# Optimization experiments

Measured on AMD Instinct MI355X. Metric: run time of the kernel, lower is better.

Reference implementation:

```python
import jax, jax.numpy as jnp
import numpy as np
from jax import lax

B, N, FD, D, H, LH, HC, NC = 8, 1024, 34, 64, 4, 128, 193, 9
STEPS, ET = 4, 2
DH = D // H
LHH = LH // 2  # hidden per LSTM direction
SCALE = float(1.0 / np.sqrt(DH))
BN_INV = float(1.0 / np.sqrt(1.0 + 1e-5))  # BatchNorm eval with running var=1


def layernorm(x, g, b, eps=1e-5):
    m = x.mean(-1, keepdims=True)
    v = ((x - m) ** 2).mean(-1, keepdims=True)
    return (x - m) / jnp.sqrt(v + eps) * g + b


def mha(q_in, kv, w, b, ow, ob):
    # torch nn.MultiheadAttention, batch_first, eval (no dropout)
    wq, wk, wv = jnp.split(w, 3, 0)
    bq, bk, bv = jnp.split(b, 3, 0)
    q = (q_in @ wq.T + bq).reshape(B, N, H, DH)
    k = (kv @ wk.T + bk).reshape(B, N, H, DH)
    v = (kv @ wv.T + bv).reshape(B, N, H, DH)
    s = jnp.einsum('bqhd,bkhd->bhqk', q, k) * SCALE
    a = jax.nn.softmax(s, -1)
    o = jnp.einsum('bhqk,bkhd->bqhd', a, v).reshape(B, N, D)
    return o @ ow.T + ob


def gru(x, h, wih, whh, bih, bhh):
    gi = x @ wih.T + bih
    gh = h @ whh.T + bhh
    ir, iz, inn = jnp.split(gi, 3, -1)
    hr, hz, hn = jnp.split(gh, 3, -1)
    r = jax.nn.sigmoid(ir + hr)
    z = jax.nn.sigmoid(iz + hz)
    n = jnp.tanh(inn + r * hn)
    return (1.0 - z) * n + z * h


def lstm_dir(x, wih, whh, b, reverse):
    hd = wih.shape[0] // 4
    def step(carry, xt):
        h, c = carry
        g = xt @ wih.T + h @ whh.T + b
        i, f, gg, o = jnp.split(g, 4, -1)
        c = jax.nn.sigmoid(f) * c + jax.nn.sigmoid(i) * jnp.tanh(gg)
        h = jax.nn.sigmoid(o) * jnp.tanh(c)
        return (h, c), h
    xs = jnp.swapaxes(x, 0, 1)
    if reverse:
        xs = xs[::-1]
    z0 = jnp.zeros((x.shape[0], hd), x.dtype)
    (hf, _), hs = lax.scan(step, (z0, z0), xs)
    if reverse:
        hs = hs[::-1]
    return jnp.swapaxes(hs, 0, 1), hf


def forward(node_features, adj_data, adj_control, handcrafted_features,
            ip_w, ip_b, et_w, mha_in_w, mha_in_b, mha_out_w, mha_out_b,
            eta_w1, eta_b1, eta_w2, eta_b2, gru_wih, gru_whh, gru_bih, gru_bhh,
            ln_g, ln_b, oln_g, oln_b,
            l0f_wih, l0f_whh, l0f_b, l0b_wih, l0b_whh, l0b_b,
            l1f_wih, l1f_whh, l1f_b, l1b_wih, l1b_whh, l1b_b,
            attn_w1, attn_b1, attn_w2, attn_b2,
            hc_w1, hc_b1, bn1_g, bn1_b, hc_w2, hc_b2, bn2_g, bn2_b, hc_w3, hc_b3,
            cls_w1, cls_b1, cls_w2, cls_b2, cls_w3, cls_b3,
            topo_order, node_mask, seq_lengths):
    # input projection
    h = jax.nn.relu(node_features @ ip_w.T + ip_b)
    adjs = (adj_data, adj_control)
    for l in range(STEPS):
        msgs = []
        for e in range(ET):
            ht = h @ et_w[l, e].T
            m = mha(h, ht, mha_in_w[l, e], mha_in_b[l, e], mha_out_w[l, e], mha_out_b[l, e])
            msgs.append(jnp.einsum('bij,bjd->bid', adjs[e], m))
        st = jnp.stack(msgs, 2)            # [B,N,ET,D]
        ctx = st.mean(2)
        ai = jnp.concatenate([h, ctx], -1)
        etw = jax.nn.softmax(jax.nn.relu(ai @ eta_w1[l].T + eta_b1[l]) @ eta_w2[l].T + eta_b2[l], -1)
        messages = (st * etw[..., None]).sum(2)
        hn = gru(messages, h, gru_wih[l], gru_whh[l], gru_bih[l], gru_bhh[l])
        hn = layernorm(hn, ln_g[l], ln_b[l])
        h = layernorm(h + hn, oln_g[l], oln_b[l])
    h = h * node_mask.astype(h.dtype)[..., None]
    h_ord = jnp.take_along_axis(h, topo_order[..., None], 1)
    # 2-layer BiLSTM
    o0f, _ = lstm_dir(h_ord, l0f_wih, l0f_whh, l0f_b, False)
    o0b, _ = lstm_dir(h_ord, l0b_wih, l0b_whh, l0b_b, True)
    o0 = jnp.concatenate([o0f, o0b], -1)
    o1f, h1f = lstm_dir(o0, l1f_wih, l1f_whh, l1f_b, False)
    o1b, h1b = lstm_dir(o0, l1b_wih, l1b_whh, l1b_b, True)
    h_all = jnp.concatenate([o1f, o1b], -1)    # [B,N,LH]
    final = jnp.concatenate([h1f, h1b], -1)    # [B,LH]
    # masked attention pooling
    scores = (jnp.tanh(h_all @ attn_w1.T + attn_b1) @ attn_w2.T + attn_b2)[..., 0]
    smask = jnp.arange(N)[None, :] < seq_lengths[:, None]
    aw = jax.nn.softmax(jnp.where(smask, scores, -1e9), -1)
    pooled = jnp.einsum('bt,btd->bd', aw, h_all)
    comb = pooled + final
    # handcrafted encoder (BN in eval mode, running stats 0/1)
    x = jax.nn.relu(handcrafted_features @ hc_w1.T + hc_b1)
    x = x * BN_INV * bn1_g + bn1_b
    x = jax.nn.relu(x @ hc_w2.T + hc_b2)
    x = x * BN_INV * bn2_g + bn2_b
    x = jax.nn.relu(x @ hc_w3.T + hc_b3)
    hf = jnp.concatenate([comb, x], -1)
    y = jax.nn.relu(hf @ cls_w1.T + cls_b1)
    y = jax.nn.relu(y @ cls_w2.T + cls_b2)
    return y @ cls_w3.T + cls_b3


def setup_inputs():
    key = jax.random.key(0)
    ks = iter(jax.random.split(key, 128))
    def rn(shape, s=0.05):
        return (jax.random.normal(next(ks), shape) * s).astype(jnp.float32)
    inp = {}
    inp['node_features'] = jax.random.normal(next(ks), (B, N, FD), jnp.float32)
    inp['adj_data'] = jax.random.uniform(next(ks), (B, N, N), jnp.float32) * (2.0 / N)
    inp['adj_control'] = jax.random.uniform(next(ks), (B, N, N), jnp.float32) * (2.0 / N)
    inp['handcrafted_features'] = jax.random.normal(next(ks), (B, HC), jnp.float32)
    inp['ip_w'] = rn((D, FD)); inp['ip_b'] = rn((D,))
    inp['et_w'] = rn((STEPS, ET, D, D))
    inp['mha_in_w'] = rn((STEPS, ET, 3 * D, D)); inp['mha_in_b'] = rn((STEPS, ET, 3 * D))
    inp['mha_out_w'] = rn((STEPS, ET, D, D)); inp['mha_out_b'] = rn((STEPS, ET, D))
    inp['eta_w1'] = rn((STEPS, D, 2 * D)); inp['eta_b1'] = rn((STEPS, D))
    inp['eta_w2'] = rn((STEPS, ET, D)); inp['eta_b2'] = rn((STEPS, ET))
    inp['gru_wih'] = rn((STEPS, 3 * D, D)); inp['gru_whh'] = rn((STEPS, 3 * D, D))
    inp['gru_bih'] = rn((STEPS, 3 * D)); inp['gru_bhh'] = rn((STEPS, 3 * D))
    inp['ln_g'] = jnp.ones((STEPS, D), jnp.float32); inp['ln_b'] = jnp.zeros((STEPS, D), jnp.float32)
    inp['oln_g'] = jnp.ones((STEPS, D), jnp.float32); inp['oln_b'] = jnp.zeros((STEPS, D), jnp.float32)
    inp['l0f_wih'] = rn((4 * LHH, D)); inp['l0f_whh'] = rn((4 * LHH, LHH)); inp['l0f_b'] = rn((4 * LHH,))
    inp['l0b_wih'] = rn((4 * LHH, D)); inp['l0b_whh'] = rn((4 * LHH, LHH)); inp['l0b_b'] = rn((4 * LHH,))
    inp['l1f_wih'] = rn((4 * LHH, LH)); inp['l1f_whh'] = rn((4 * LHH, LHH)); inp['l1f_b'] = rn((4 * LHH,))
    inp['l1b_wih'] = rn((4 * LHH, LH)); inp['l1b_whh'] = rn((4 * LHH, LHH)); inp['l1b_b'] = rn((4 * LHH,))
    inp['attn_w1'] = rn((64, LH)); inp['attn_b1'] = rn((64,))
    inp['attn_w2'] = rn((1, 64)); inp['attn_b2'] = rn((1,))
    inp['hc_w1'] = rn((256, HC)); inp['hc_b1'] = rn((256,))
    inp['bn1_g'] = jnp.ones((256,), jnp.float32); inp['bn1_b'] = jnp.zeros((256,), jnp.float32)
    inp['hc_w2'] = rn((128, 256)); inp['hc_b2'] = rn((128,))
    inp['bn2_g'] = jnp.ones((128,), jnp.float32); inp['bn2_b'] = jnp.zeros((128,), jnp.float32)
    inp['hc_w3'] = rn((64, 128)); inp['hc_b3'] = rn((64,))
    inp['cls_w1'] = rn((128, LH + 64)); inp['cls_b1'] = rn((128,))
    inp['cls_w2'] = rn((64, 128)); inp['cls_b2'] = rn((64,))
    inp['cls_w3'] = rn((NC, 64)); inp['cls_b3'] = rn((NC,))
    inp['topo_order'] = jax.vmap(lambda k: jax.random.permutation(k, N))(jax.random.split(next(ks), B))
    inp['node_mask'] = jnp.ones((B, N), bool)
    inp['seq_lengths'] = jax.random.randint(next(ks), (B,), N // 2, N + 1)
    return inp


def reference(node_features, adj_data, adj_control, handcrafted_features,
              ip_w, ip_b, et_w, mha_in_w, mha_in_b, mha_out_w, mha_out_b,
              eta_w1, eta_b1, eta_w2, eta_b2, gru_wih, gru_whh, gru_bih, gru_bhh,
              ln_g, ln_b, oln_g, oln_b,
              l0f_wih, l0f_whh, l0f_b, l0b_wih, l0b_whh, l0b_b,
              l1f_wih, l1f_whh, l1f_b, l1b_wih, l1b_whh, l1b_b,
              attn_w1, attn_b1, attn_w2, attn_b2,
              hc_w1, hc_b1, bn1_g, bn1_b, hc_w2, hc_b2, bn2_g, bn2_b, hc_w3, hc_b3,
              cls_w1, cls_b1, cls_w2, cls_b2, cls_w3, cls_b3,
              topo_order, node_mask, seq_lengths):
    return forward(node_features, adj_data, adj_control, handcrafted_features,
                   ip_w, ip_b, et_w, mha_in_w, mha_in_b, mha_out_w, mha_out_b,
                   eta_w1, eta_b1, eta_w2, eta_b2, gru_wih, gru_whh, gru_bih, gru_bhh,
                   ln_g, ln_b, oln_g, oln_b,
                   l0f_wih, l0f_whh, l0f_b, l0b_wih, l0b_whh, l0b_b,
                   l1f_wih, l1f_whh, l1f_b, l1b_wih, l1b_whh, l1b_b,
                   attn_w1, attn_b1, attn_w2, attn_b2,
                   hc_w1, hc_b1, bn1_g, bn1_b, hc_w2, hc_b2, bn2_g, bn2_b, hc_w3, hc_b3,
                   cls_w1, cls_b1, cls_w2, cls_b2, cls_w3, cls_b3,
                   topo_order, node_mask, seq_lengths)
```

## Files before the change

kernel.cpp:

```cpp
#include <hip/hip_runtime.h>
#include <math.h>

#define NB 8
#define NN 1024
#define NT 8192
#define SCALE_C 0.25f
#define BN_INV_C 0.99999500003749969f
#define LN_EPS 1e-5f

typedef __attribute__((ext_vector_type(8))) short bf16x8;
typedef __attribute__((ext_vector_type(4))) float f32x4;

__device__ __forceinline__ float sigmoidf_(float x){ return 1.f/(1.f+__expf(-x)); }
__device__ __forceinline__ float tanhf_(float x){
  float ax = fabsf(x);
  float e = __expf(-2.f*ax);
  float t = (1.f-e)/(1.f+e);
  return x < 0.f ? -t : t;
}
__device__ __forceinline__ float wsum64(float v){
  #pragma unroll
  for (int m=1; m<64; m<<=1) v += __shfl_xor(v, m);
  return v;
}
__device__ __forceinline__ unsigned short f2bf(float f){
  unsigned int u = __float_as_uint(f);
  unsigned int r = (u + 0x7fffu + ((u>>16)&1u)) >> 16;
  return (unsigned short)r;
}

__global__ __launch_bounds__(256) void gemm_tn(
    const float* __restrict__ A, long aZ,
    const float* __restrict__ W, long wZ,
    const float* __restrict__ Bias, long bZ,
    float* __restrict__ C, long cZ,
    int M, int Ncols, int K, int act)
{
  const int z = blockIdx.z;
  A += (long)z * aZ; W += (long)z * wZ; C += (long)z * cZ;
  if (Bias) Bias += (long)z * bZ;
  const int m0 = blockIdx.x * 64;
  const int n0 = blockIdx.y * 64;
  const int tid = threadIdx.x;
  __shared__ float As[16][68];
  __shared__ float Ws[16][68];
  const int lm = tid >> 2;
  const int kq = (tid & 3) * 4;
  const int tr = tid >> 4;
  const int tc = tid & 15;
  float acc[4][4] = {};
  const bool v16 = ((K & 15) == 0);
  for (int kt = 0; kt < K; kt += 16) {
    if (v16) {
      float4 a = *reinterpret_cast<const float4*>(&A[(long)(m0 + lm) * K + kt + kq]);
      As[kq+0][lm]=a.x; As[kq+1][lm]=a.y; As[kq+2][lm]=a.z; As[kq+3][lm]=a.w;
      float4 w = *reinterpret_cast<const float4*>(&W[(long)(n0 + lm) * K + kt + kq]);
      Ws[kq+0][lm]=w.x; Ws[kq+1][lm]=w.y; Ws[kq+2][lm]=w.z; Ws[kq+3][lm]=w.w;
    } else {
      #pragma unroll
      for (int j = 0; j < 4; ++j) {
        int k = kt + kq + j;
        As[kq+j][lm] = (k < K) ? A[(long)(m0+lm)*K + k] : 0.f;
        Ws[kq+j][lm] = (k < K) ? W[(long)(n0+lm)*K + k] : 0.f;
      }
    }
    __syncthreads();
    #pragma unroll
    for (int k = 0; k < 16; ++k) {
      float4 av = *reinterpret_cast<const float4*>(&As[k][tr*4]);
      float4 wv = *reinterpret_cast<const float4*>(&Ws[k][tc*4]);
      float a_[4] = {av.x,av.y,av.z,av.w};
      float w_[4] = {wv.x,wv.y,wv.z,wv.w};
      #pragma unroll
      for (int i=0;i<4;++i)
        #pragma unroll
        for (int j=0;j<4;++j) acc[i][j] += a_[i]*w_[j];
    }
    __syncthreads();
  }
  #pragma unroll
  for (int i=0;i<4;++i) {
    const long m = m0 + tr*4 + i;
    #pragma unroll
    for (int j=0;j<4;++j) {
      const int n = n0 + tc*4 + j;
      float v = acc[i][j];
      if (Bias) v += Bias[n];
      if (act) v = fmaxf(v, 0.f);
      C[m*Ncols + n] = v;
    }
  }
}

__global__ __launch_bounds__(256) void wprep(
    const float* __restrict__ miw, const float* __restrict__ etw,
    float* __restrict__ wcomb)
{
  const int le = blockIdx.x;
  const float* Wm = miw + (long)le*192*64;
  const float* Et = etw + (long)le*64*64;
  float* Out = wcomb + (long)le*192*64;
  __shared__ float es[64][65];
  const int tid = threadIdx.x;
  for (int i = tid; i < 4096; i += 256) es[i>>6][i&63] = Et[i];
  __syncthreads();
  for (int i = tid; i < 4096; i += 256) Out[i] = Wm[i];
  for (int i = tid; i < 8192; i += 256) {
    const int r = 64 + (i >> 6), d = i & 63;
    const float* wr = &Wm[(long)r*64];
    float a = 0.f;
    #pragma unroll 8
    for (int c = 0; c < 64; ++c) a += wr[c] * es[c][d];
    Out[(long)r*64 + d] = a;
  }
}

__global__ __launch_bounds__(256) void mcvt_kernel(
    const float* __restrict__ m0, const float* __restrict__ m1,
    unsigned short* __restrict__ mmT)
{
  const int e = blockIdx.y;
  const float* src = e ? m1 : m0;
  unsigned short* dst = mmT + (long)e*64*8192;
  const int r0 = blockIdx.x * 64;
  __shared__ unsigned short tile[64][65];
  const int tid = threadIdx.x;
  const int lr = tid >> 2, c0 = (tid & 3) * 16;
  #pragma unroll
  for (int i = 0; i < 16; i += 4) {
    float4 v = *reinterpret_cast<const float4*>(&src[(long)(r0+lr)*64 + c0 + i]);
    tile[lr][c0+i+0] = f2bf(v.x);
    tile[lr][c0+i+1] = f2bf(v.y);
    tile[lr][c0+i+2] = f2bf(v.z);
    tile[lr][c0+i+3] = f2bf(v.w);
  }
  __syncthreads();
  const int n = tid >> 2, rr = (tid & 3) * 16;
  #pragma unroll
  for (int i = 0; i < 16; i += 4) {
    ushort4 w;
    w.x = tile[rr+i+0][n];
    w.y = tile[rr+i+1][n];
    w.z = tile[rr+i+2][n];
    w.w = tile[rr+i+3][n];
    *reinterpret_cast<ushort4*>(&dst[(long)n*8192 + r0 + rr + i]) = w;
  }
}

__global__ __launch_bounds__(256) void gemm_nn_mfma(
    const float* __restrict__ adjD, const float* __restrict__ adjC,
    const unsigned short* __restrict__ mmT,
    float* __restrict__ msg)
{
  const int z = blockIdx.z;
  const int e = z >> 3, b = z & 7;
  const float* A = (e ? adjC : adjD) + (long)b*NN*NN;
  const unsigned short* Bt = mmT + (long)e*64*8192 + (long)b*NN;
  float* Cp = msg + ((long)e*NT + (long)b*NN) * 64;
  const int tid = threadIdx.x;
  const int w = tid >> 6;
  const int l = tid & 63;
  const int r = l & 15;
  const int kg = l >> 4;
  const long arow = (long)(blockIdx.x*64 + w*16 + r) * NN;

  f32x4 acc0 = {0.f,0.f,0.f,0.f}, acc1 = acc0, acc2 = acc0, acc3 = acc0;

  for (int k0 = 0; k0 < NN; k0 += 32) {
    const float4* ap = reinterpret_cast<const float4*>(&A[arow + k0 + kg*8]);
    float4 a0 = ap[0], a1 = ap[1];
    union { unsigned short us[8]; bf16x8 v; } au;
    au.us[0]=f2bf(a0.x); au.us[1]=f2bf(a0.y); au.us[2]=f2bf(a0.z); au.us[3]=f2bf(a0.w);
    au.us[4]=f2bf(a1.x); au.us[5]=f2bf(a1.y); au.us[6]=f2bf(a1.z); au.us[7]=f2bf(a1.w);
    bf16x8 b0 = *reinterpret_cast<const bf16x8*>(&Bt[(long)(0*16+r)*8192 + k0 + kg*8]);
    bf16x8 b1 = *reinterpret_cast<const bf16x8*>(&Bt[(long)(1*16+r)*8192 + k0 + kg*8]);
    bf16x8 b2 = *reinterpret_cast<const bf16x8*>(&Bt[(long)(2*16+r)*8192 + k0 + kg*8]);
    bf16x8 b3 = *reinterpret_cast<const bf16x8*>(&Bt[(long)(3*16+r)*8192 + k0 + kg*8]);
    acc0 = __builtin_amdgcn_mfma_f32_16x16x32_bf16(au.v, b0, acc0, 0, 0, 0);
    acc1 = __builtin_amdgcn_mfma_f32_16x16x32_bf16(au.v, b1, acc1, 0, 0, 0);
    acc2 = __builtin_amdgcn_mfma_f32_16x16x32_bf16(au.v, b2, acc2, 0, 0, 0);
    acc3 = __builtin_amdgcn_mfma_f32_16x16x32_bf16(au.v, b3, acc3, 0, 0, 0);
  }
  const int crow = blockIdx.x*64 + w*16 + kg*4;
  #pragma unroll
  for (int i = 0; i < 4; ++i) {
    Cp[(long)(crow+i)*64 + 0*16 + r] = acc0[i];
    Cp[(long)(crow+i)*64 + 1*16 + r] = acc1[i];
    Cp[(long)(crow+i)*64 + 2*16 + r] = acc2[i];
    Cp[(long)(crow+i)*64 + 3*16 + r] = acc3[i];
  }
}

__global__ __launch_bounds__(256) void attn_kernel(
    const float* __restrict__ qkv, float* __restrict__ O)
{
  const int e = blockIdx.z;
  const float* base = qkv + (long)e*1572864;
  float* o = O + (long)e*524288;
  const int bh = blockIdx.y;
  const int b = bh >> 2, head = bh & 3;
  const int q0 = blockIdx.x * 64;
  const int tid = threadIdx.x;
  const int r = tid >> 2, p = tid & 3;
  const long row = (long)b*NN + q0 + r;
  float qreg[16];
  {
    const float4* qp = reinterpret_cast<const float4*>(&base[row*192 + head*16]);
    #pragma unroll
    for (int i=0;i<4;++i) {
      float4 v = qp[i];
      qreg[4*i+0]=v.x*SCALE_C; qreg[4*i+1]=v.y*SCALE_C;
      qreg[4*i+2]=v.z*SCALE_C; qreg[4*i+3]=v.w*SCALE_C;
    }
  }
  float mx = -1e30f, ssum = 0.f, acc[16];
  #pragma unroll
  for (int d=0;d<16;++d) acc[d]=0.f;
  __shared__ float ks[128][17];
  __shared__ float vs[128][17];
  for (int j0 = 0; j0 < NN; j0 += 128) {
    {
      const int jr = tid >> 1;
      const int hf = (tid & 1) * 8;
      const long rr = ((long)b*NN + j0 + jr)*192 + head*16 + hf;
      const float4* kp = reinterpret_cast<const float4*>(&base[rr + 64]);
      float4 k0 = kp[0], k1 = kp[1];
      ks[jr][hf+0]=k0.x; ks[jr][hf+1]=k0.y; ks[jr][hf+2]=k0.z; ks[jr][hf+3]=k0.w;
      ks[jr][hf+4]=k1.x; ks[jr][hf+5]=k1.y; ks[jr][hf+6]=k1.z; ks[jr][hf+7]=k1.w;
      const float4* vp = reinterpret_cast<const float4*>(&base[rr + 128]);
      float4 v0 = vp[0], v1 = vp[1];
      vs[jr][hf+0]=v0.x; vs[jr][hf+1]=v0.y; vs[jr][hf+2]=v0.z; vs[jr][hf+3]=v0.w;
      vs[jr][hf+4]=v1.x; vs[jr][hf+5]=v1.y; vs[jr][hf+6]=v1.z; vs[jr][hf+7]=v1.w;
    }
    __syncthreads();
    for (int jj = p; jj < 128; jj += 4) {
      float s = 0.f;
      #pragma unroll
      for (int d=0;d<16;++d) s += qreg[d]*ks[jj][d];
      if (s <= mx) {
        float ee = __expf(s - mx);
        ssum += ee;
        #pragma unroll
        for (int d=0;d<16;++d) acc[d] += ee*vs[jj][d];
      } else {
        float cc = __expf(mx - s);
        ssum = ssum*cc + 1.f;
        #pragma unroll
        for (int d=0;d<16;++d) acc[d] = acc[d]*cc + vs[jj][d];
        mx = s;
      }
    }
    __syncthreads();
  }
  #pragma unroll
  for (int mask=1; mask<=2; mask<<=1) {
    float om = __shfl_xor(mx, mask);
    float os = __shfl_xor(ssum, mask);
    float nm = fmaxf(mx, om);
    float c1 = __expf(mx-nm), c2 = __expf(om-nm);
    ssum = ssum*c1 + os*c2;
    #pragma unroll
    for (int d=0;d<16;++d) {
      float ov = __shfl_xor(acc[d], mask);
      acc[d] = acc[d]*c1 + ov*c2;
    }
    mx = nm;
  }
  if (p == 0) {
    float inv = 1.f/ssum;
    float4* op = reinterpret_cast<float4*>(&o[row*64 + head*16]);
    #pragma unroll
    for (int i=0;i<4;++i) {
      float4 v;
      v.x=acc[4*i+0]*inv; v.y=acc[4*i+1]*inv; v.z=acc[4*i+2]*inv; v.w=acc[4*i+3]*inv;
      op[i] = v;
    }
  }
}

__global__ __launch_bounds__(64) void fused_gate_gru_ln(
    float* __restrict__ h, const float* __restrict__ msg0, const float* __restrict__ msg1,
    const float* __restrict__ ew1, const float* __restrict__ eb1,
    const float* __restrict__ ew2, const float* __restrict__ eb2,
    const float* __restrict__ wih, const float* __restrict__ whh,
    const float* __restrict__ bih, const float* __restrict__ bhh,
    const float* __restrict__ lng, const float* __restrict__ lnb,
    const float* __restrict__ olng, const float* __restrict__ olnb)
{
  const int r0 = blockIdx.x * 4;
  const int tid = threadIdx.x;
  __shared__ float hsm[4][64], m0s[4][64], m1s[4][64], tss[4][64];
  #pragma unroll
  for (int r=0;r<4;++r) {
    hsm[r][tid] = h[(long)(r0+r)*64 + tid];
    m0s[r][tid] = msg0[(long)(r0+r)*64 + tid];
    m1s[r][tid] = msg1[(long)(r0+r)*64 + tid];
  }
  __syncthreads();
  float ta[4] = {0.f,0.f,0.f,0.f};
  for (int k=0;k<64;++k) {
    float w = ew1[tid*128 + k];
    #pragma unroll
    for (int r=0;r<4;++r) ta[r] += w * hsm[r][k];
  }
  for (int k=0;k<64;++k) {
    float w = ew1[tid*128 + 64 + k];
    #pragma unroll
    for (int r=0;r<4;++r) ta[r] += w * 0.5f*(m0s[r][k]+m1s[r][k]);
  }
  #pragma unroll
  for (int r=0;r<4;++r) tss[r][tid] = fmaxf(ta[r] + eb1[tid], 0.f);
  __syncthreads();
  const float w2a = ew2[tid], w2b = ew2[64+tid];
  #pragma unroll
  for (int r=0;r<4;++r) {
    float l0 = wsum64(tss[r][tid]*w2a) + eb2[0];
    float l1 = wsum64(tss[r][tid]*w2b) + eb2[1];
    float mm = fmaxf(l0,l1);
    float e0 = __expf(l0-mm), e1 = __expf(l1-mm);
    float wgt0 = e0/(e0+e1);
    m0s[r][tid] = wgt0*m0s[r][tid] + (1.f-wgt0)*m1s[r][tid];
  }
  __syncthreads();
  float air[4]={},aiz[4]={},ain[4]={},ahr[4]={},ahz[4]={},ahn[4]={};
  for (int k=0;k<64;++k) {
    float wir = wih[(long)tid*64 + k];
    float wiz = wih[(long)(64+tid)*64 + k];
    float win = wih[(long)(128+tid)*64 + k];
    float whr = whh[(long)tid*64 + k];
    float whz = whh[(long)(64+tid)*64 + k];
    float whn = whh[(long)(128+tid)*64 + k];
    #pragma unroll
    for (int r=0;r<4;++r) {
      float x = m0s[r][k], hh = hsm[r][k];
      air[r] += wir*x; aiz[r] += wiz*x; ain[r] += win*x;
      ahr[r] += whr*hh; ahz[r] += whz*hh; ahn[r] += whn*hh;
    }
  }
  const float bir = bih[tid], biz = bih[64+tid], bin_ = bih[128+tid];
  const float bhr = bhh[tid], bhz = bhh[64+tid], bhn = bhh[128+tid];
  const float g1 = lng[tid], b1v = lnb[tid], g2 = olng[tid], b2v = olnb[tid];
  #pragma unroll
  for (int r=0;r<4;++r) {
    float rg = sigmoidf_(air[r]+bir + ahr[r]+bhr);
    float zg = sigmoidf_(aiz[r]+biz + ahz[r]+bhz);
    float ng = tanhf_(ain[r]+bin_ + rg*(ahn[r]+bhn));
    float hnv = (1.f-zg)*ng + zg*hsm[r][tid];
    float mu = wsum64(hnv) * 0.015625f;
    float dv = hnv - mu;
    float var = wsum64(dv*dv) * 0.015625f;
    float y = dv * rsqrtf(var + LN_EPS) * g1 + b1v;
    float ho = hsm[r][tid] + y;
    float mu2 = wsum64(ho) * 0.015625f;
    float d2 = ho - mu2;
    float var2 = wsum64(d2*d2) * 0.015625f;
    h[(long)(r0+r)*64 + tid] = d2 * rsqrtf(var2 + LN_EPS) * g2 + b2v;
  }
}

__global__ __launch_bounds__(256) void permute_kernel(
    const float* __restrict__ h, const int* __restrict__ topo, float* __restrict__ ho)
{
  const long idx = (long)blockIdx.x*256 + threadIdx.x;
  const int row = (int)(idx >> 6), d = (int)(idx & 63);
  const int b = row >> 10, i = row & 1023;
  const int src = topo[b*1024 + i];
  ho[idx] = h[((long)b*1024 + src)*64 + d];
}

__global__ __launch_bounds__(256) void lstm_seq(
    const float* __restrict__ xpF, const float* __restrict__ xpB,
    const float* __restrict__ whhF, const float* __restrict__ whhB,
    float* __restrict__ out)
{
  const int b = blockIdx.x;
  const int dir = blockIdx.y;
  const float* xp = dir ? xpB : xpF;
  const float* W  = dir ? whhB : whhF;
  const int colOff = dir * 64;
  const int tid = threadIdx.x;
  const int wv  = tid >> 6;
  const int j   = tid & 63;

  float4 wreg[16];
  {
    const float4* wp = reinterpret_cast<const float4*>(&W[tid*64]);
    #pragma unroll
    for (int i=0;i<16;++i) wreg[i] = wp[i];
  }

  __shared__ __align__(16) float hs[2][64];
  __shared__ float g5[2][320];
  float c = 0.f;
  if (tid < 64) hs[0][tid] = 0.f;

  int ts = dir ? (NN-1) : 0;
  float xnext = xp[((long)b*NN + ts)*256 + tid];
  __syncthreads();

  int p = 0;
  for (int t = 0; t < NN; ++t) {
    const int cur = ts;
    const float x = xnext;
    if (t + 1 < NN) {
      ts = dir ? (NN-2-t) : (t+1);
      xnext = xp[((long)b*NN + ts)*256 + tid];
    }
    float a0 = x, a1 = 0.f, a2 = 0.f, a3 = 0.f;
    #pragma unroll
    for (int k=0;k<16;k+=4) {
      float4 h0 = *reinterpret_cast<const float4*>(&hs[p][k*4]);
      float4 h1 = *reinterpret_cast<const float4*>(&hs[p][k*4+4]);
      float4 h2 = *reinterpret_cast<const float4*>(&hs[p][k*4+8]);
      float4 h3 = *reinterpret_cast<const float4*>(&hs[p][k*4+12]);
      a0 += wreg[k].x*h0.x + wreg[k].y*h0.y + wreg[k].z*h0.z + wreg[k].w*h0.w;
      a1 += wreg[k+1].x*h1.x + wreg[k+1].y*h1.y + wreg[k+1].z*h1.z + wreg[k+1].w*h1.w;
      a2 += wreg[k+2].x*h2.x + wreg[k+2].y*h2.y + wreg[k+2].z*h2.z + wreg[k+2].w*h2.w;
      a3 += wreg[k+3].x*h3.x + wreg[k+3].y*h3.y + wreg[k+3].z*h3.z + wreg[k+3].w*h3.w;
    }
    float dot = (a0+a1)+(a2+a3);
    float v = (wv == 2) ? tanhf_(dot) : sigmoidf_(dot);
    g5[p][j*5 + wv] = v;
    __syncthreads();
    const float gi = g5[p][j*5+0];
    const float gf = g5[p][j*5+1];
    const float gg = g5[p][j*5+2];
    const float go = g5[p][j*5+3];
    c = gf*c + gi*gg;
    const float hval = go * tanhf_(c);
    hs[p^1][j] = hval;
    if (tid < 64) out[((long)b*NN + cur)*128 + colOff + j] = hval;
    p ^= 1;
  }
}

__global__ __launch_bounds__(64) void score_kernel(
    const float* __restrict__ h_all, const float* __restrict__ w1,
    const float* __restrict__ b1, const float* __restrict__ w2,
    const float* __restrict__ b2, float* __restrict__ scores)
{
  const int row = blockIdx.x, tid = threadIdx.x;
  __shared__ float xs[128];
  xs[tid]    = h_all[(long)row*128 + tid];
  xs[64+tid] = h_all[(long)row*128 + 64 + tid];
  __syncthreads();
  float a = b1[tid];
  for (int k=0;k<128;++k) a += w1[tid*128+k]*xs[k];
  float s = tanhf_(a) * w2[tid];
  s = wsum64(s);
  if (tid==0) scores[row] = s + b2[0];
}

__global__ __launch_bounds__(256) void pool_kernel(
    const float* __restrict__ h_all, const float* __restrict__ scores,
    const int* __restrict__ seqlen, float* __restrict__ comb)
{
  const int b = blockIdx.x, tid = threadIdx.x;
  __shared__ float aw[1024];
  __shared__ float red[4];
  __shared__ float part[256];
  const int L = seqlen[b];
  float mx = -1e30f;
  for (int t = tid; t < 1024; t += 256) {
    float s = (t < L) ? scores[b*1024+t] : -1e30f;
    aw[t] = s;
    mx = fmaxf(mx, s);
  }
  #pragma unroll
  for (int m=1;m<64;m<<=1) mx = fmaxf(mx, __shfl_xor(mx,m));
  if ((tid&63)==0) red[tid>>6] = mx;
  __syncthreads();
  mx = fmaxf(fmaxf(red[0],red[1]), fmaxf(red[2],red[3]));
  __syncthreads();
  float ss = 0.f;
  for (int t = tid; t < 1024; t += 256) {
    float e = (t < L) ? __expf(aw[t]-mx) : 0.f;
    aw[t] = e; ss += e;
  }
  ss = wsum64(ss);
  if ((tid&63)==0) red[tid>>6] = ss;
  __syncthreads();
  ss = red[0]+red[1]+red[2]+red[3];
  const float inv = 1.f/ss;
  const int d = tid & 127, hseg = tid >> 7;
  float acc = 0.f;
  for (int t = hseg; t < 1024; t += 2)
    acc += aw[t] * h_all[((long)b*1024 + t)*128 + d];
  part[tid] = acc;
  __syncthreads();
  if (tid < 128) {
    float pooled = (part[tid] + part[tid+128]) * inv;
    float fin = (tid < 64) ? h_all[((long)b*1024 + 1023)*128 + tid]
                           : h_all[((long)b*1024 + 0)*128 + tid];
    comb[b*128 + tid] = pooled + fin;
  }
}

__global__ __launch_bounds__(256) void head_kernel(
    const float* __restrict__ comb, const float* __restrict__ hcf,
    const float* __restrict__ w1, const float* __restrict__ b1,
    const float* __restrict__ bn1g, const float* __restrict__ bn1b,
    const float* __restrict__ w2, const float* __restrict__ b2,
    const float* __restrict__ bn2g, const float* __restrict__ bn2b,
    const float* __restrict__ w3, const float* __restrict__ b3,
    const float* __restrict__ cw1, const float* __restrict__ cb1,
    const float* __restrict__ cw2, const float* __restrict__ cb2,
    const float* __restrict__ cw3, const float* __restrict__ cb3,
    float* __restrict__ outp)
{
  const int b = blockIdx.x, tid = threadIdx.x;
  __shared__ float hrow[193];
  __shared__ float x1[256], x2[128], hf[192], y1[128], y2[64];
  if (tid < 193) hrow[tid] = hcf[b*193 + tid];
  if (tid < 128) hf[tid] = comb[b*128 + tid];
  __syncthreads();
  {
    float a = b1[tid];
    for (int k=0;k<193;++k) a += w1[(long)tid*193+k]*hrow[k];
    x1[tid] = fmaxf(a,0.f)*BN_INV_C*bn1g[tid] + bn1b[tid];
  }
  __syncthreads();
  if (tid < 128) {
    float a = b2[tid];
    for (int k=0;k<256;++k) a += w2[(long)tid*256+k]*x1[k];
    x2[tid] = fmaxf(a,0.f)*BN_INV_C*bn2g[tid] + bn2b[tid];
  }
  __syncthreads();
  if (tid < 64) {
    float a = b3[tid];
    for (int k=0;k<128;++k) a += w3[(long)tid*128+k]*x2[k];
    hf[128+tid] = fmaxf(a,0.f);
  }
  __syncthreads();
  if (tid < 128) {
    float a = cb1[tid];
    for (int k=0;k<192;++k) a += cw1[(long)tid*192+k]*hf[k];
    y1[tid] = fmaxf(a,0.f);
  }
  __syncthreads();
  if (tid < 64) {
    float a = cb2[tid];
    for (int k=0;k<128;++k) a += cw2[(long)tid*128+k]*y1[k];
    y2[tid] = fmaxf(a,0.f);
  }
  __syncthreads();
  if (tid < 9) {
    float a = cb3[tid];
    for (int k=0;k<64;++k) a += cw3[(long)tid*64+k]*y2[k];
    outp[b*9+tid] = a;
  }
}

extern "C" void kernel_launch(void* const* d_in, const int* in_sizes, int n_in,
                              void* d_out, int out_size, void* d_ws, size_t ws_size,
                              hipStream_t stream)
{
  const float* nf   = (const float*)d_in[0];
  const float* adjD = (const float*)d_in[1];
  const float* adjC = (const float*)d_in[2];
  const float* hcf  = (const float*)d_in[3];
  const float* ip_w = (const float*)d_in[4];
  const float* ip_b = (const float*)d_in[5];
  const float* et_w = (const float*)d_in[6];
  const float* miw  = (const float*)d_in[7];
  const float* mib  = (const float*)d_in[8];
  const float* mow  = (const float*)d_in[9];
  const float* mob  = (const float*)d_in[10];
  const float* ew1  = (const float*)d_in[11];
  const float* eb1  = (const float*)d_in[12];
  const float* ew2  = (const float*)d_in[13];
  const float* eb2  = (const float*)d_in[14];
  const float* gwih = (const float*)d_in[15];
  const float* gwhh = (const float*)d_in[16];
  const float* gbih = (const float*)d_in[17];
  const float* gbhh = (const float*)d_in[18];
  const float* lng  = (const float*)d_in[19];
  const float* lnb  = (const float*)d_in[20];
  const float* olng = (const float*)d_in[21];
  const float* olnb = (const float*)d_in[22];
  const float* l0f_wih = (const float*)d_in[23];
  const float* l0f_whh = (const float*)d_in[24];
  const float* l0f_b   = (const float*)d_in[25];
  const float* l0b_wih = (const float*)d_in[26];
  const float* l0b_whh = (const float*)d_in[27];
  const float* l0b_b   = (const float*)d_in[28];
  const float* l1f_wih = (const float*)d_in[29];
  const float* l1f_whh = (const float*)d_in[30];
  const float* l1f_b   = (const float*)d_in[31];
  const float* l1b_wih = (const float*)d_in[32];
  const float* l1b_whh = (const float*)d_in[33];
  const float* l1b_b   = (const float*)d_in[34];
  const float* aw1  = (const float*)d_in[35];
  const float* ab1  = (const float*)d_in[36];
  const float* aw2  = (const float*)d_in[37];
  const float* ab2  = (const float*)d_in[38];
  const float* hw1  = (const float*)d_in[39];
  const float* hb1  = (const float*)d_in[40];
  const float* bn1g = (const float*)d_in[41];
  const float* bn1b = (const float*)d_in[42];
  const float* hw2  = (const float*)d_in[43];
  const float* hb2  = (const float*)d_in[44];
  const float* bn2g = (const float*)d_in[45];
  const float* bn2b = (const float*)d_in[46];
  const float* hw3  = (const float*)d_in[47];
  const float* hb3  = (const float*)d_in[48];
  const float* cw1  = (const float*)d_in[49];
  const float* cb1  = (const float*)d_in[50];
  const float* cw2  = (const float*)d_in[51];
  const float* cb2  = (const float*)d_in[52];
  const float* cw3  = (const float*)d_in[53];
  const float* cb3  = (const float*)d_in[54];
  const int*  topo  = (const int*)d_in[55];
  const int*  seqlen= (const int*)d_in[57];

  float* ws = (float*)d_ws;
  float* h     = ws;
  float* qkv   = ws + 524288;
  float* ob    = ws + 3670016;
  float* mbuf  = ws + 4718592;
  float* msg   = ws + 5767168;
  unsigned short* mmT = (unsigned short*)(ws + 6815744);
  float* wcomb = ws + 7340032;
  float* hord  = ws + 524288;
  float* xpf   = ws + 1048576;
  float* xpb   = ws + 3145728;
  float* o0    = ws + 5767168;
  float* hall  = ws + 7438336;
  float* sc    = ws + 8486912;
  float* comb  = ws + 8495104;

  dim3 blk(256);

  wprep<<<dim3(8), blk, 0, stream>>>(miw, et_w, wcomb);

  gemm_tn<<<dim3(128,1,1), blk, 0, stream>>>(nf,0, ip_w,0, ip_b,0, h,0, NT,64,34, 1);

  for (int l=0; l<4; ++l) {
    const float* mowl = mow + (size_t)l*2*64*64;
    const float* mobl = mob + (size_t)l*2*64;
    gemm_tn<<<dim3(128,3,2), blk, 0, stream>>>(h,0, wcomb + (size_t)l*2*12288, 12288,
                                               mib + (size_t)l*2*192, 192,
                                               qkv, 1572864, NT,192,64, 0);
    attn_kernel<<<dim3(16,32,2), blk, 0, stream>>>(qkv, ob);
    gemm_tn<<<dim3(128,1,2), blk, 0, stream>>>(ob,524288, mowl,4096, mobl,64, mbuf,524288, NT,64,64, 0);
    mcvt_kernel<<<dim3(128,2), blk, 0, stream>>>(mbuf, mbuf+524288, mmT);
    gemm_nn_mfma<<<dim3(16,1,16), blk, 0, stream>>>(adjD, adjC, mmT, msg);
    fused_gate_gru_ln<<<dim3(2048), dim3(64), 0, stream>>>(h, msg, msg+524288,
        ew1 + (size_t)l*64*128, eb1 + l*64, ew2 + l*128, eb2 + l*2,
        gwih + (size_t)l*192*64, gwhh + (size_t)l*192*64, gbih + l*192, gbhh + l*192,
        lng + l*64, lnb + l*64, olng + l*64, olnb + l*64);
  }

  permute_kernel<<<dim3(2048), blk, 0, stream>>>(h, topo, hord);

  gemm_tn<<<dim3(128,4,1), blk, 0, stream>>>(hord,0, l0f_wih,0, l0f_b,0, xpf,0, NT,256,64, 0);
  gemm_tn<<<dim3(128,4,1), blk, 0, stream>>>(hord,0, l0b_wih,0, l0b_b,0, xpb,0, NT,256,64, 0);
  lstm_seq<<<dim3(8,2), blk, 0, stream>>>(xpf, xpb, l0f_whh, l0b_whh, o0);
  gemm_tn<<<dim3(128,4,1), blk, 0, stream>>>(o0,0, l1f_wih,0, l1f_b,0, xpf,0, NT,256,128, 0);
  gemm_tn<<<dim3(128,4,1), blk, 0, stream>>>(o0,0, l1b_wih,0, l1b_b,0, xpb,0, NT,256,128, 0);
  lstm_seq<<<dim3(8,2), blk, 0, stream>>>(xpf, xpb, l1f_whh, l1b_whh, hall);

  score_kernel<<<dim3(8192), dim3(64), 0, stream>>>(hall, aw1, ab1, aw2, ab2, sc);
  pool_kernel<<<dim3(8), blk, 0, stream>>>(hall, sc, seqlen, comb);
  head_kernel<<<dim3(8), blk, 0, stream>>>(comb, hcf,
      hw1,hb1,bn1g,bn1b, hw2,hb2,bn2g,bn2b, hw3,hb3,
      cw1,cb1, cw2,cb2, cw3,cb3, (float*)d_out);
}
```

Baseline: 2.780 ms.

## Batch all sequences per LSTM direction into one block using fp16 MFMA recurrence

The LSTM recurrence kernel now runs one block per direction and processes all 8 batch sequences together. The hidden-to-gate product becomes fp16 16x16x32 MFMA operations, with weights held in registers as fp16 and the hidden state kept in a swizzled fp16 LDS buffer. This removes the per-step scalar FMA dot products and the gate-exchange LDS round trip, and each thread now handles all four gates for its units. The costs are fp16 rounding of the weights and hidden state in a 1024-step recurrence, and only 2 blocks running on the whole GPU.

```diff
diff --git a/kernel.cpp b/kernel.cpp
--- a/kernel.cpp
+++ b/kernel.cpp
@@ -10,6 +10,7 @@
 
 typedef __attribute__((ext_vector_type(8))) short bf16x8;
 typedef __attribute__((ext_vector_type(4))) float f32x4;
+typedef _Float16 f16x8 __attribute__((ext_vector_type(8)));
 
 __device__ __forceinline__ float sigmoidf_(float x){ return 1.f/(1.f+__expf(-x)); }
 __device__ __forceinline__ float tanhf_(float x){
@@ -373,63 +374,93 @@
     const float* __restrict__ whhF, const float* __restrict__ whhB,
     float* __restrict__ out)
 {
-  const int b = blockIdx.x;
-  const int dir = blockIdx.y;
+  const int dir = blockIdx.x;
   const float* xp = dir ? xpB : xpF;
   const float* W  = dir ? whhB : whhF;
   const int colOff = dir * 64;
   const int tid = threadIdx.x;
-  const int wv  = tid >> 6;
-  const int j   = tid & 63;
-
-  float4 wreg[16];
+  const int w   = tid >> 6;
+  const int l   = tid & 63;
+  const int col = l & 15;
+  const int bidx = col & 7;
+  const int kg  = l >> 4;
+  const int u0  = w*16 + kg*4;
+
+  f16x8 Wf[4][2];
+  #pragma unroll
+  for (int c=0;c<4;++c)
+    #pragma unroll
+    for (int s=0;s<2;++s) {
+      const float* wr = &W[(long)(c*64 + w*16 + col)*64 + s*32 + kg*8];
+      f16x8 f;
+      #pragma unroll
+      for (int j=0;j<8;++j) f[j] = (_Float16)wr[j];
+      Wf[c][s] = f;
+    }
+
+  __shared__ __align__(16) _Float16 hbuf[2][1024];
+  for (int i = tid; i < 1024; i += 256) hbuf[0][i] = (_Float16)0.f;
+  float cst[4] = {0.f,0.f,0.f,0.f};
+
+  const int swz    = (col & 7) << 4;
+  const int rdoff0 = col*128 + ((0*64 + kg*16) ^ swz);
+  const int rdoff1 = col*128 + ((1*64 + kg*16) ^ swz);
+  const int wroff  = col*128 + ((u0*2)        ^ swz);
+
+  int ts = dir ? (NN-1) : 0;
+  float4 xq[4];
   {
-    const float4* wp = reinterpret_cast<const float4*>(&W[tid*64]);
-    #pragma unroll
-    for (int i=0;i<16;++i) wreg[i] = wp[i];
-  }
-
-  __shared__ __align__(16) float hs[2][64];
-  __shared__ float g5[2][320];
-  float c = 0.f;
-  if (tid < 64) hs[0][tid] = 0.f;
-
-  int ts = dir ? (NN-1) : 0;
-  float xnext = xp[((long)b*NN + ts)*256 + tid];
+    const float* xr = &xp[((long)bidx*NN + ts)*256];
+    #pragma unroll
+    for (int c=0;c<4;++c)
+      xq[c] = *reinterpret_cast<const float4*>(&xr[c*64 + u0]);
+  }
   __syncthreads();
 
   int p = 0;
   for (int t = 0; t < NN; ++t) {
     const int cur = ts;
-    const float x = xnext;
+    const char* hb = (const char*)(&hbuf[p][0]);
+    f16x8 B0 = *reinterpret_cast<const f16x8*>(hb + rdoff0);
+    f16x8 B1 = *reinterpret_cast<const f16x8*>(hb + rdoff1);
+    f32x4 aI = {xq[0].x, xq[0].y, xq[0].z, xq[0].w};
+    f32x4 aF = {xq[1].x, xq[1].y, xq[1].z, xq[1].w};
+    f32x4 aG = {xq[2].x, xq[2].y, xq[2].z, xq[2].w};
+    f32x4 aO = {xq[3].x, xq[3].y, xq[3].z, xq[3].w};
     if (t + 1 < NN) {
       ts = dir ? (NN-2-t) : (t+1);
-      xnext = xp[((long)b*NN + ts)*256 + tid];
-    }
-    float a0 = x, a1 = 0.f, a2 = 0.f, a3 = 0.f;
-    #pragma unroll
-    for (int k=0;k<16;k+=4) {
-      float4 h0 = *reinterpret_cast<const float4*>(&hs[p][k*4]);
-      float4 h1 = *reinterpret_cast<const float4*>(&hs[p][k*4+4]);
-      float4 h2 = *reinterpret_cast<const float4*>(&hs[p][k*4+8]);
-      float4 h3 = *reinterpret_cast<const float4*>(&hs[p][k*4+12]);
-      a0 += wreg[k].x*h0.x + wreg[k].y*h0.y + wreg[k].z*h0.z + wreg[k].w*h0.w;
-      a1 += wreg[k+1].x*h1.x + wreg[k+1].y*h1.y + wreg[k+1].z*h1.z + wreg[k+1].w*h1.w;
-      a2 += wreg[k+2].x*h2.x + wreg[k+2].y*h2.y + wreg[k+2].z*h2.z + wreg[k+2].w*h2.w;
-      a3 += wreg[k+3].x*h3.x + wreg[k+3].y*h3.y + wreg[k+3].z*h3.z + wreg[k+3].w*h3.w;
-    }
-    float dot = (a0+a1)+(a2+a3);
-    float v = (wv == 2) ? tanhf_(dot) : sigmoidf_(dot);
-    g5[p][j*5 + wv] = v;
+      const float* xr = &xp[((long)bidx*NN + ts)*256];
+      #pragma unroll
+      for (int c=0;c<4;++c)
+        xq[c] = *reinterpret_cast<const float4*>(&xr[c*64 + u0]);
+    }
+    aI = __builtin_amdgcn_mfma_f32_16x16x32_f16(Wf[0][0], B0, aI, 0, 0, 0);
+    aF = __builtin_amdgcn_mfma_f32_16x16x32_f16(Wf[1][0], B0, aF, 0, 0, 0);
+    aG = __builtin_amdgcn_mfma_f32_16x16x32_f16(Wf[2][0], B0, aG, 0, 0, 0);
+    aO = __builtin_amdgcn_mfma_f32_16x16x32_f16(Wf[3][0], B0, aO, 0, 0, 0);
+    aI = __builtin_amdgcn_mfma_f32_16x16x32_f16(Wf[0][1], B1, aI, 0, 0, 0);
+    aF = __builtin_amdgcn_mfma_f32_16x16x32_f16(Wf[1][1], B1, aF, 0, 0, 0);
+    aG = __builtin_amdgcn_mfma_f32_16x16x32_f16(Wf[2][1], B1, aG, 0, 0, 0);
+    aO = __builtin_amdgcn_mfma_f32_16x16x32_f16(Wf[3][1], B1, aO, 0, 0, 0);
+
+    float hv[4];
+    union { _Float16 h4[4]; uint2 u2; } pk;
+    #pragma unroll
+    for (int i=0;i<4;++i) {
+      const float ig = sigmoidf_(aI[i]);
+      const float fg = sigmoidf_(aF[i]);
+      const float gg = tanhf_(aG[i]);
+      const float og = sigmoidf_(aO[i]);
+      cst[i] = fg*cst[i] + ig*gg;
+      hv[i] = og * tanhf_(cst[i]);
+      pk.h4[i] = (_Float16)hv[i];
+    }
+    *reinterpret_cast<uint2*>(((char*)(&hbuf[p^1][0])) + wroff) = pk.u2;
+    if (col < 8) {
+      float4 o4; o4.x=hv[0]; o4.y=hv[1]; o4.z=hv[2]; o4.w=hv[3];
+      *reinterpret_cast<float4*>(&out[((long)bidx*NN + cur)*128 + colOff + u0]) = o4;
+    }
     __syncthreads();
-    const float gi = g5[p][j*5+0];
-    const float gf = g5[p][j*5+1];
-    const float gg = g5[p][j*5+2];
-    const float go = g5[p][j*5+3];
-    c = gf*c + gi*gg;
-    const float hval = go * tanhf_(c);
-    hs[p^1][j] = hval;
-    if (tid < 64) out[((long)b*NN + cur)*128 + colOff + j] = hval;
     p ^= 1;
   }
 }
@@ -655,10 +686,10 @@
 
   gemm_tn<<<dim3(128,4,1), blk, 0, stream>>>(hord,0, l0f_wih,0, l0f_b,0, xpf,0, NT,256,64, 0);
   gemm_tn<<<dim3(128,4,1), blk, 0, stream>>>(hord,0, l0b_wih,0, l0b_b,0, xpb,0, NT,256,64, 0);
-  lstm_seq<<<dim3(8,2), blk, 0, stream>>>(xpf, xpb, l0f_whh, l0b_whh, o0);
+  lstm_seq<<<dim3(2), blk, 0, stream>>>(xpf, xpb, l0f_whh, l0b_whh, o0);
   gemm_tn<<<dim3(128,4,1), blk, 0, stream>>>(o0,0, l1f_wih,0, l1f_b,0, xpf,0, NT,256,128, 0);
   gemm_tn<<<dim3(128,4,1), blk, 0, stream>>>(o0,0, l1b_wih,0, l1b_b,0, xpb,0, NT,256,128, 0);
-  lstm_seq<<<dim3(8,2), blk, 0, stream>>>(xpf, xpb, l1f_whh, l1b_whh, hall);
+  lstm_seq<<<dim3(2), blk, 0, stream>>>(xpf, xpb, l1f_whh, l1b_whh, hall);
 
   score_kernel<<<dim3(8192), dim3(64), 0, stream>>>(hall, aw1, ab1, aw2, ab2, sc);
   pool_kernel<<<dim3(8), blk, 0, stream>>>(hall, sc, seqlen, comb);
```

After: 3.404 ms. 22.4% more time.

## Prefetch LSTM input projections via deep async global-to-LDS ring

Applied to the files above, without the earlier changes.

The single-step register prefetch of the input projection in the sequential LSTM kernel is replaced by an 8-deep ring of asynchronous global-to-LDS loads, with hand-placed vmcnt waits. The full __syncthreads is replaced by an LDS-only wait plus a raw s_barrier, so the per-step barrier no longer drains outstanding global loads and stores. The aim is to keep global memory latency off the serial 1024-step critical path. This relies on vmcnt accounting staying correct with the interleaved output stores, and adds 16 KB of LDS per block.

```diff
diff --git a/kernel.cpp b/kernel.cpp
--- a/kernel.cpp
+++ b/kernel.cpp
@@ -368,7 +368,7 @@
   ho[idx] = h[((long)b*1024 + src)*64 + d];
 }
 
-__global__ __launch_bounds__(256) void lstm_seq(
+__global__ __launch_bounds__(256, 1) void lstm_seq(
     const float* __restrict__ xpF, const float* __restrict__ xpB,
     const float* __restrict__ whhF, const float* __restrict__ whhB,
     float* __restrict__ out)
@@ -391,21 +391,34 @@
 
   __shared__ __align__(16) float hs[2][64];
   __shared__ float g5[2][320];
+  __shared__ __align__(16) float ring[16][256];
   float c = 0.f;
   if (tid < 64) hs[0][tid] = 0.f;
-
-  int ts = dir ? (NN-1) : 0;
-  float xnext = xp[((long)b*NN + ts)*256 + tid];
-  __syncthreads();
+  __syncthreads();
+
+  const long rowb = (long)b*NN;
+  #pragma unroll
+  for (int s = 0; s < 8; ++s) {
+    const int ts = dir ? (NN-1-s) : s;
+    __builtin_amdgcn_global_load_lds(
+        (const __attribute__((address_space(1))) void*)(&xp[(rowb + ts)*256 + tid]),
+        (__attribute__((address_space(3))) void*)(&ring[s][wv*64]), 4, 0, 0);
+  }
 
   int p = 0;
   for (int t = 0; t < NN; ++t) {
-    const int cur = ts;
-    const float x = xnext;
-    if (t + 1 < NN) {
-      ts = dir ? (NN-2-t) : (t+1);
-      xnext = xp[((long)b*NN + ts)*256 + tid];
-    }
+    const int cur = dir ? (NN-1-t) : t;
+    if (t + 8 < NN) {
+      asm volatile("s_waitcnt vmcnt(7)" ::: "memory");
+      const int ts2 = dir ? (NN-9-t) : (t+8);
+      __builtin_amdgcn_global_load_lds(
+          (const __attribute__((address_space(1))) void*)(&xp[(rowb + ts2)*256 + tid]),
+          (__attribute__((address_space(3))) void*)(&ring[(t+8)&15][wv*64]), 4, 0, 0);
+    } else {
+      asm volatile("s_waitcnt vmcnt(0)" ::: "memory");
+    }
+    const float x = ring[t & 15][tid];
+
     float a0 = x, a1 = 0.f, a2 = 0.f, a3 = 0.f;
     #pragma unroll
     for (int k=0;k<16;k+=4) {
@@ -421,7 +434,8 @@
     float dot = (a0+a1)+(a2+a3);
     float v = (wv == 2) ? tanhf_(dot) : sigmoidf_(dot);
     g5[p][j*5 + wv] = v;
-    __syncthreads();
+    asm volatile("s_waitcnt lgkmcnt(0)" ::: "memory");
+    __builtin_amdgcn_s_barrier();
     const float gi = g5[p][j*5+0];
     const float gf = g5[p][j*5+1];
     const float gg = g5[p][j*5+2];
@@ -429,7 +443,7 @@
     c = gf*c + gi*gg;
     const float hval = go * tanhf_(c);
     hs[p^1][j] = hval;
-    if (tid < 64) out[((long)b*NN + cur)*128 + colOff + j] = hval;
+    if (tid < 64) out[(rowb + cur)*128 + colOff + j] = hval;
     p ^= 1;
   }
 }
```

Result: slower. 3.224 ms (+16.0%).
